# Performance work log

Measured on AMD Instinct MI355X. Metric: run time of the kernel, lower is better.

## Reference

```python
import jax, jax.numpy as jnp
import numpy as np

N_NODES = 100000
N_EDGES = 1600000
IN_DIM = 64
HID = 64
N_LAYERS = 2
BN_EPS = 1e-5


def setup_inputs() -> dict:
    key = jax.random.key(0)
    ks = jax.random.split(key, 10)
    s = 0.02
    return {
        "x": jax.random.normal(ks[0], (N_NODES, IN_DIM), dtype=jnp.float32),
        "edge_index": jax.random.randint(ks[1], (2, N_EDGES), 0, N_NODES),
        "edge_attr": jax.random.uniform(ks[2], (N_EDGES,), dtype=jnp.float32),
        "lin_W": jax.random.normal(ks[3], (IN_DIM, HID), dtype=jnp.float32) * s,
        "lin_b": jnp.zeros((HID,), dtype=jnp.float32),
        "eenc_w": jax.random.normal(ks[4], (HID,), dtype=jnp.float32) * s,
        "eenc_b": jnp.zeros((HID,), dtype=jnp.float32),
        "conv_W": jax.random.normal(ks[5], (N_LAYERS, HID, HID), dtype=jnp.float32) * s,
        "conv_b": jnp.zeros((N_LAYERS, HID), dtype=jnp.float32),
        "bn_gamma": jnp.ones((N_LAYERS, HID), dtype=jnp.float32),
        "bn_beta": jnp.zeros((N_LAYERS, HID), dtype=jnp.float32),
    }


def _forward(x, edge_index, edge_attr, lin_W, lin_b, eenc_w, eenc_b,
             conv_W, conv_b, bn_gamma, bn_beta):
    n = x.shape[0]
    src, dst = edge_index[0], edge_index[1]
    # input projection (in_dim > 1 -> lin_layer branch)
    h = x @ lin_W + lin_b                                  # [N, HID]
    e = edge_attr[:, None] * eenc_w[None, :] + eenc_b      # [E, HID]
    h0 = h
    h = h.at[src].set(jax.nn.relu(h0[src] + e))
    h = h.at[dst].set(jax.nn.relu(h0[dst] + e))
    # GCN normalization with self-loops (weight 1), shared across layers
    loops = jnp.arange(n)
    s2 = jnp.concatenate([src, loops])
    d2 = jnp.concatenate([dst, loops])
    w2 = jnp.concatenate([edge_attr, jnp.ones((n,), dtype=h.dtype)])
    deg = jax.ops.segment_sum(w2, d2, num_segments=n)
    dinv = jnp.where(deg > 0, 1.0 / jnp.sqrt(jnp.where(deg > 0, deg, 1.0)), 0.0)
    norm = dinv[s2] * w2 * dinv[d2]                        # [E+N]
    h_list = []
    for l in range(N_LAYERS):
        xw = h @ conv_W[l]                                 # [N, HID]
        agg = jax.ops.segment_sum(norm[:, None] * xw[s2], d2, num_segments=n)
        agg = agg + conv_b[l]
        mean = jnp.mean(agg, axis=0)
        var = jnp.mean((agg - mean) ** 2, axis=0)          # biased, as BN uses
        hn = (agg - mean) / jnp.sqrt(var + BN_EPS) * bn_gamma[l] + bn_beta[l]
        # dropout is identity (eval mode); relu on all but last layer
        h = hn if l == N_LAYERS - 1 else jax.nn.relu(hn)
        h_list.append(h)
    return jnp.concatenate(h_list, axis=1)                 # [N, N_LAYERS*HID]


def reference(x, edge_index, edge_attr, lin_W, lin_b, eenc_w, eenc_b,
              conv_W, conv_b, bn_gamma, bn_beta):
    return _forward(x, edge_index, edge_attr, lin_W, lin_b, eenc_w, eenc_b,
                    conv_W, conv_b, bn_gamma, bn_beta)
```

## Files before the change

kernel.cpp:

```cpp
#include <hip/hip_runtime.h>
#include <hip/hip_fp16.h>

#define N_NODES 100000
#define N_EDGES 1600000
#define BN_EPS 1e-5f
#define NBLK_E 6250
#define NBLK_G 3125
#define NBLK_N 391
#define NBINS 391
#define BCAP 4608
#define PT 4096
#define NPART 391
#define OVF_CAP 32768
#define A18 262144.0f
#define A18_INV 3.814697265625e-6f
typedef unsigned long long ull;
typedef unsigned int uint;


__global__ void init_kernel(int* gcnt, int* win, uint* zbitmap, int* flags, float* bnacc) {
    int v = blockIdx.x * blockDim.x + threadIdx.x;
    if (v < N_NODES) win[v] = -1;
    if (v < NBINS) gcnt[v] = 0;
    if (v < 3125) zbitmap[v] = 0;
    if (v < 2) flags[v] = 0;
    if (v < 256) bnacc[v] = 0.0f;
}

__launch_bounds__(256)
__global__ void partition_gemm(const int* __restrict__ src, const int* __restrict__ dst,
                               const float* __restrict__ attr,
                               ull* __restrict__ bucket, int* __restrict__ gcnt,
                               int* __restrict__ flags, int* __restrict__ ovf_b,
                               ull* __restrict__ ovf_e,
                               const float* __restrict__ x, const float* __restrict__ lin_W,
                               const float* __restrict__ lin_b, float* __restrict__ h0) {
    __shared__ ull ent[PT];
    __shared__ unsigned short ebin[PT];
    __shared__ int hist[NBINS];
    __shared__ int cur[NBINS];
    __shared__ int gdel[NBINS];
    __shared__ int sc[512];
    int t = threadIdx.x;
    if (blockIdx.x < NPART) {
        int e0 = blockIdx.x * PT;
        int n = N_EDGES - e0; if (n > PT) n = PT;
        for (int b = t; b < NBINS; b += 256) hist[b] = 0;
        __syncthreads();
        for (int k = t; k < n; k += 256) atomicAdd(&hist[dst[e0 + k] >> 8], 1);
        __syncthreads();
        sc[t] = (t < NBINS) ? hist[t] : 0;
        sc[t + 256] = (t + 256 < NBINS) ? hist[t + 256] : 0;
        __syncthreads();
        for (int off = 1; off < 512; off <<= 1) {
            int a0 = sc[t] + ((t >= off) ? sc[t - off] : 0);
            int a1 = sc[t + 256] + sc[t + 256 - off];
            __syncthreads();
            sc[t] = a0; sc[t + 256] = a1;
            __syncthreads();
        }
        for (int b = t; b < NBINS; b += 256) {
            int lb = sc[b] - hist[b];
            cur[b] = lb;
            int gb = atomicAdd(&gcnt[b], hist[b]);
            gdel[b] = gb - lb;
        }
        __syncthreads();
        for (int k = t; k < n; k += 256) {
            int i = e0 + k;
            int d = dst[i];
            uint aq = (uint)(attr[i] * A18); if (aq > 0x3FFFFu) aq = 0x3FFFFu;
            int bin = d >> 8;
            ull e = ((ull)(d & 255) << 56) | ((ull)i << 35) | ((ull)src[i] << 18) | aq;
            int p = atomicAdd(&cur[bin], 1);
            ent[p] = e;
            ebin[p] = (unsigned short)bin;
        }
        __syncthreads();
        for (int k = t; k < n; k += 256) {
            int b = ebin[k];
            int off = k + gdel[b];
            if (off < BCAP) bucket[(size_t)b * BCAP + off] = ent[k];
            else {
                int q = atomicAdd(&flags[1], 1);
                if (q < OVF_CAP) { ovf_b[q] = b; ovf_e[q] = ent[k]; }
            }
        }
        return;
    }
    float* xs = (float*)ent;
    int lane = t & 63, w = t >> 6;
    int base = (blockIdx.x - NPART) * 32;
    const float4* Xv = (const float4*)(x + (size_t)base * 64);
    float4* xsv = (float4*)xs;
    xsv[t] = Xv[t];
    xsv[t + 256] = Xv[t + 256];
    float wc[64];
    #pragma unroll
    for (int k = 0; k < 64; ++k) wc[k] = lin_W[k * 64 + lane];
    __syncthreads();
    float bval = lin_b[lane];
    for (int rr = 0; rr < 8; ++rr) {
        int rl = w * 8 + rr;
        float acc = bval;
        #pragma unroll
        for (int k = 0; k < 64; ++k) acc = fmaf(xs[rl * 64 + k], wc[k], acc);
        h0[(size_t)(base + rl) * 64 + lane] = acc;
    }
}

__launch_bounds__(256)
__global__ void finalize_reorder(const ull* __restrict__ bucket, const int* __restrict__ gcnt,
                                 const int* __restrict__ ovf_b, const ull* __restrict__ ovf_e,
                                 int* __restrict__ flags, uint* __restrict__ zbitmap,
                                 float* __restrict__ dinv, float* __restrict__ wa,
                                 ull* __restrict__ csr2, int* __restrict__ startv,
                                 int* __restrict__ lenv) {
    __shared__ ull ent[BCAP];
    __shared__ int cnt[256];
    __shared__ int sc[256];
    __shared__ int cur[256];
    __shared__ int cbase[257];
    int t = threadIdx.x, b = blockIdx.x;
    int len = gcnt[b], blen = len < BCAP ? len : BCAP;
    const ull* bb = bucket + (size_t)b * BCAP;
    cnt[t] = 0;
    __syncthreads();
    ull r[18];
    #pragma unroll
    for (int k = 0; k < 18; ++k) {
        int j = k * 256 + t;
        r[k] = 0;
        if (j < blen) {
            ull e = bb[j];
            r[k] = e;
            atomicAdd(&cnt[(int)(e >> 56)], 1);
        }
    }
    __syncthreads();
    sc[t] = cnt[t];
    __syncthreads();
    for (int off = 1; off < 256; off <<= 1) {
        int a = sc[t] + ((t >= off) ? sc[t - off] : 0);
        __syncthreads();
        sc[t] = a;
        __syncthreads();
    }
    cbase[t + 1] = sc[t];
    if (t == 0) cbase[0] = 0;
    cur[t] = sc[t] - cnt[t];
    __syncthreads();
    #pragma unroll
    for (int k = 0; k < 18; ++k) {
        int j = k * 256 + t;
        if (j < blen) {
            ull e = r[k];
            int p = atomicAdd(&cur[(int)(e >> 56)], 1);
            ent[p] = e;
        }
    }
    __syncthreads();
    size_t base = (size_t)b * BCAP;
    for (int k = t; k < blen; k += 256) {
        ull e = ent[k];
        csr2[base + k] = (((ull)(e & 0x3FFFFull)) << 32) | ((e >> 18) & 0x1FFFFull);
    }
    int j0 = cbase[t], j1 = cbase[t + 1];
    float sum = 0.0f; uint winx = 0, wat = 0;
    for (int j = j0; j < j1; ++j) {
        ull e = ent[j];
        uint aq = (uint)(e & 0x3FFFFull);
        sum += (float)aq * A18_INV;
        uint ei = (uint)((e >> 35) & 0x1FFFFFull) + 1u;
        if (ei > winx) { winx = ei; wat = aq; }
    }
    if (len > BCAP) {
        int oc = flags[1]; if (oc > OVF_CAP) oc = OVF_CAP;
        for (int q = 0; q < oc; ++q) {
            if (ovf_b[q] != b) continue;
            ull e = ovf_e[q];
            if ((int)(e >> 56) != t) continue;
            uint aq = (uint)(e & 0x3FFFFull);
            sum += (float)aq * A18_INV;
            uint ei = (uint)((e >> 35) & 0x1FFFFFull) + 1u;
            if (ei > winx) { winx = ei; wat = aq; }
        }
    }
    int v = b * 256 + t;
    if (v < N_NODES) {
        dinv[v] = rsqrtf(1.0f + sum);
        startv[v] = (int)(base + j0);
        lenv[v] = j1 - j0;
        if (winx > 0) {
            wa[v] = (float)wat * A18_INV;
        } else {
            wa[v] = -1.0f;
            atomicOr(&zbitmap[v >> 5], 1u << (v & 31));
            flags[0] = 1;
        }
    }
}

__global__ void fixup_scan(const int* __restrict__ src, const int* __restrict__ flags,
                           const uint* __restrict__ zbitmap, int* __restrict__ win) {
    if (flags[0] == 0) return;
    int i = blockIdx.x * 256 + threadIdx.x;
    int s = src[i];
    if ((zbitmap[s >> 5] >> (s & 31)) & 1u) atomicMax(&win[s], i);
}

__global__ void fixup_apply(const int* __restrict__ flags, const uint* __restrict__ zbitmap,
                            const int* __restrict__ win, const float* __restrict__ attr,
                            float* __restrict__ wa) {
    if (flags[0] == 0) return;
    int v = blockIdx.x * 256 + threadIdx.x;
    if (v >= N_NODES) return;
    if (((zbitmap[v >> 5] >> (v & 31)) & 1u) && win[v] >= 0) wa[v] = attr[win[v]];
}

__launch_bounds__(256)
__global__ void gemm_l0_nrm(const float* __restrict__ h0, const float* __restrict__ W,
                            const float* __restrict__ wa, const float* __restrict__ ew,
                            const float* __restrict__ eb, __half* __restrict__ xw16,
                            ull* __restrict__ csr2, const int* __restrict__ gcnt,
                            const float* __restrict__ dinv) {
    __shared__ float xs[2048];
    int t = threadIdx.x;
    if (blockIdx.x < NBINS) {
        int b = blockIdx.x;
        int len = gcnt[b], blen = len < BCAP ? len : BCAP;
        ull* c = csr2 + (size_t)b * BCAP;
        for (int k = t; k < blen; k += 256) {
            ull pk = c[k];
            uint s = (uint)pk;
            float np = (float)(uint)(pk >> 32) * A18_INV * dinv[s];
            c[k] = ((ull)__float_as_uint(np) << 32) | s;
        }
        return;
    }
    int lane = t & 63, w = t >> 6;
    int base = (blockIdx.x - NBINS) * 32;
    const float4* Hv = (const float4*)(h0 + (size_t)base * 64);
    #pragma unroll
    for (int q = 0; q < 2; ++q) {
        int idx = t + q * 256;
        int rl = idx >> 4, f0 = (idx & 15) * 4;
        float4 v = Hv[idx];
        float wav = wa[base + rl];
        if (wav >= 0.0f) {
            v.x = fmaxf(fmaf(wav, ew[f0 + 0], v.x + eb[f0 + 0]), 0.0f);
            v.y = fmaxf(fmaf(wav, ew[f0 + 1], v.y + eb[f0 + 1]), 0.0f);
            v.z = fmaxf(fmaf(wav, ew[f0 + 2], v.z + eb[f0 + 2]), 0.0f);
            v.w = fmaxf(fmaf(wav, ew[f0 + 3], v.w + eb[f0 + 3]), 0.0f);
        }
        ((float4*)xs)[idx] = v;
    }
    float wc[64];
    #pragma unroll
    for (int k = 0; k < 64; ++k) wc[k] = W[k * 64 + lane];
    __syncthreads();
    for (int rr = 0; rr < 8; ++rr) {
        int rl = w * 8 + rr;
        float acc = 0.0f;
        #pragma unroll
        for (int k = 0; k < 64; ++k) acc = fmaf(xs[rl * 64 + k], wc[k], acc);
        xw16[(size_t)(base + rl) * 64 + lane] = __float2half(acc);
    }
}

__launch_bounds__(256)
__global__ void gemm_l1(const float* __restrict__ agg, const float* __restrict__ bnacc,
                        const float* __restrict__ gamma, const float* __restrict__ beta,
                        const float* __restrict__ W, float* __restrict__ out,
                        __half* __restrict__ xw16) {
    __shared__ float xs[2048];
    int t = threadIdx.x, lane = t & 63, w = t >> 6;
    int base = blockIdx.x * 32;
    const float4* Av = (const float4*)(agg + (size_t)base * 64);
    const float invN = 1.0f / (float)N_NODES;
    #pragma unroll
    for (int q = 0; q < 2; ++q) {
        int idx = t + q * 256;
        int rl = idx >> 4, f0 = (idx & 15) * 4;
        float4 v = Av[idx];
        float vv[4] = {v.x, v.y, v.z, v.w};
        #pragma unroll
        for (int c = 0; c < 4; ++c) {
            int f = f0 + c;
            float mean = bnacc[f] * invN;
            float var = bnacc[64 + f] * invN - mean * mean;
            float scl = gamma[f] * rsqrtf(var + BN_EPS);
            float bs = beta[f] - mean * scl;
            vv[c] = fmaxf(fmaf(vv[c], scl, bs), 0.0f);
        }
        float4 r = {vv[0], vv[1], vv[2], vv[3]};
        ((float4*)xs)[idx] = r;
        *(float4*)(out + (size_t)(base + rl) * 128 + f0) = r;
    }
    float wc[64];
    #pragma unroll
    for (int k = 0; k < 64; ++k) wc[k] = W[k * 64 + lane];
    __syncthreads();
    for (int rr = 0; rr < 8; ++rr) {
        int rl = w * 8 + rr;
        float acc = 0.0f;
        #pragma unroll
        for (int k = 0; k < 64; ++k) acc = fmaf(xs[rl * 64 + k], wc[k], acc);
        xw16[(size_t)(base + rl) * 64 + lane] = __float2half(acc);
    }
}

__launch_bounds__(256)
__global__ void gather4(const __half* __restrict__ xw16, const ull* __restrict__ csr2,
                        const int* __restrict__ startv, const int* __restrict__ lenv,
                        const float* __restrict__ dinv, const int* __restrict__ gcnt,
                        const int* __restrict__ flags, const int* __restrict__ ovf_b,
                        const ull* __restrict__ ovf_e,
                        const float* __restrict__ convb, float* __restrict__ agg,
                        float* __restrict__ bnacc) {
    __shared__ float reds[4][64];
    __shared__ float redq[4][64];
    int t = threadIdx.x, lane = t & 63, w = t >> 6;
    int ng = lane >> 4, fl = lane & 15, f0 = fl * 4, ngb = ng << 4;
    float cb0 = convb[f0], cb1 = convb[f0 + 1], cb2 = convb[f0 + 2], cb3 = convb[f0 + 3];
    float s0 = 0.f, s1 = 0.f, s2 = 0.f, s3 = 0.f;
    float q0 = 0.f, q1 = 0.f, q2 = 0.f, q3 = 0.f;
    int ovfn = flags[1];
    for (int v = blockIdx.x * 16 + w * 4 + ng; v < N_NODES; v += 32768) {
        float dv = dinv[v];
        int sb = startv[v], ln = lenv[v];
        float2 raw = *(const float2*)(xw16 + (size_t)v * 64 + f0);
        float2 xv01 = __half22float2(*(__half2*)&raw.x);
        float2 xv23 = __half22float2(*(__half2*)&raw.y);
        float w2 = dv * dv;
        float a0 = w2 * xv01.x, a1 = w2 * xv01.y, a2 = w2 * xv23.x, a3 = w2 * xv23.y;
        float b0 = 0.f, b1 = 0.f, b2 = 0.f, b3 = 0.f;
        for (int c0 = 0; c0 < ln; c0 += 16) {
            int m = ln - c0; if (m > 16) m = 16;
            ull pk = (fl < m) ? csr2[sb + c0 + fl] : 0ull;
            int j = 0;
            for (; j + 4 <= m; j += 4) {
                ull pA = __shfl(pk, ngb + j, 64);
                ull pB = __shfl(pk, ngb + j + 1, 64);
                ull pC = __shfl(pk, ngb + j + 2, 64);
                ull pD = __shfl(pk, ngb + j + 3, 64);
                float2 rA = *(const float2*)(xw16 + (size_t)(uint)pA * 64 + f0);
                float2 rB = *(const float2*)(xw16 + (size_t)(uint)pB * 64 + f0);
                float2 rC = *(const float2*)(xw16 + (size_t)(uint)pC * 64 + f0);
                float2 rD = *(const float2*)(xw16 + (size_t)(uint)pD * 64 + f0);
                float nA = __uint_as_float((uint)(pA >> 32)) * dv;
                float nB = __uint_as_float((uint)(pB >> 32)) * dv;
                float nC = __uint_as_float((uint)(pC >> 32)) * dv;
                float nD = __uint_as_float((uint)(pD >> 32)) * dv;
                float2 xA01 = __half22float2(*(__half2*)&rA.x);
                float2 xA23 = __half22float2(*(__half2*)&rA.y);
                float2 xB01 = __half22float2(*(__half2*)&rB.x);
                float2 xB23 = __half22float2(*(__half2*)&rB.y);
                float2 xC01 = __half22float2(*(__half2*)&rC.x);
                float2 xC23 = __half22float2(*(__half2*)&rC.y);
                float2 xD01 = __half22float2(*(__half2*)&rD.x);
                float2 xD23 = __half22float2(*(__half2*)&rD.y);
                a0 = fmaf(nA, xA01.x, a0); a1 = fmaf(nA, xA01.y, a1);
                a2 = fmaf(nA, xA23.x, a2); a3 = fmaf(nA, xA23.y, a3);
                b0 = fmaf(nB, xB01.x, b0); b1 = fmaf(nB, xB01.y, b1);
                b2 = fmaf(nB, xB23.x, b2); b3 = fmaf(nB, xB23.y, b3);
                a0 = fmaf(nC, xC01.x, a0); a1 = fmaf(nC, xC01.y, a1);
                a2 = fmaf(nC, xC23.x, a2); a3 = fmaf(nC, xC23.y, a3);
                b0 = fmaf(nD, xD01.x, b0); b1 = fmaf(nD, xD01.y, b1);
                b2 = fmaf(nD, xD23.x, b2); b3 = fmaf(nD, xD23.y, b3);
            }
            for (; j < m; ++j) {
                ull pA = __shfl(pk, ngb + j, 64);
                float2 rA = *(const float2*)(xw16 + (size_t)(uint)pA * 64 + f0);
                float nA = __uint_as_float((uint)(pA >> 32)) * dv;
                float2 xA01 = __half22float2(*(__half2*)&rA.x);
                float2 xA23 = __half22float2(*(__half2*)&rA.y);
                a0 = fmaf(nA, xA01.x, a0); a1 = fmaf(nA, xA01.y, a1);
                a2 = fmaf(nA, xA23.x, a2); a3 = fmaf(nA, xA23.y, a3);
            }
        }
        float t0 = a0 + b0, t1 = a1 + b1, t2 = a2 + b2, t3 = a3 + b3;
        if (ovfn > 0 && gcnt[v >> 8] > BCAP) {
            int oc = ovfn; if (oc > OVF_CAP) oc = OVF_CAP;
            int ld = v & 255, b = v >> 8;
            for (int q = 0; q < oc; ++q) {
                if (ovf_b[q] != b) continue;
                ull e = ovf_e[q];
                if ((int)(e >> 56) != ld) continue;
                uint s = (uint)((e >> 18) & 0x1FFFFull);
                float nr = (float)(uint)(e & 0x3FFFFull) * A18_INV * dinv[s] * dv;
                float2 rr = *(const float2*)(xw16 + (size_t)s * 64 + f0);
                float2 x01 = __half22float2(*(__half2*)&rr.x);
                float2 x23 = __half22float2(*(__half2*)&rr.y);
                t0 = fmaf(nr, x01.x, t0); t1 = fmaf(nr, x01.y, t1);
                t2 = fmaf(nr, x23.x, t2); t3 = fmaf(nr, x23.y, t3);
            }
        }
        t0 += cb0; t1 += cb1; t2 += cb2; t3 += cb3;
        *(float4*)(agg + (size_t)v * 64 + f0) = make_float4(t0, t1, t2, t3);
        s0 += t0; q0 += t0 * t0;
        s1 += t1; q1 += t1 * t1;
        s2 += t2; q2 += t2 * t2;
        s3 += t3; q3 += t3 * t3;
    }
    s0 += __shfl_xor(s0, 16, 64); s0 += __shfl_xor(s0, 32, 64);
    s1 += __shfl_xor(s1, 16, 64); s1 += __shfl_xor(s1, 32, 64);
    s2 += __shfl_xor(s2, 16, 64); s2 += __shfl_xor(s2, 32, 64);
    s3 += __shfl_xor(s3, 16, 64); s3 += __shfl_xor(s3, 32, 64);
    q0 += __shfl_xor(q0, 16, 64); q0 += __shfl_xor(q0, 32, 64);
    q1 += __shfl_xor(q1, 16, 64); q1 += __shfl_xor(q1, 32, 64);
    q2 += __shfl_xor(q2, 16, 64); q2 += __shfl_xor(q2, 32, 64);
    q3 += __shfl_xor(q3, 16, 64); q3 += __shfl_xor(q3, 32, 64);
    if (ng == 0) {
        reds[w][f0] = s0; reds[w][f0 + 1] = s1; reds[w][f0 + 2] = s2; reds[w][f0 + 3] = s3;
        redq[w][f0] = q0; redq[w][f0 + 1] = q1; redq[w][f0 + 2] = q2; redq[w][f0 + 3] = q3;
    }
    __syncthreads();
    if (t < 64) {
        float ss = reds[0][t] + reds[1][t] + reds[2][t] + reds[3][t];
        float qq = redq[0][t] + redq[1][t] + redq[2][t] + redq[3][t];
        atomicAdd(&bnacc[t], ss);
        atomicAdd(&bnacc[64 + t], qq);
    }
}

__launch_bounds__(256)
__global__ void bn_final(const float* __restrict__ agg, const float* __restrict__ bnacc,
                         const float* __restrict__ gamma, const float* __restrict__ beta,
                         float* __restrict__ out) {
    int idx = blockIdx.x * 256 + threadIdx.x;
    int c = idx & 63, v = idx >> 6;
    const float invN = 1.0f / (float)N_NODES;
    float mean = bnacc[c] * invN;
    float var = bnacc[64 + c] * invN - mean * mean;
    float scl = gamma[c] * rsqrtf(var + BN_EPS);
    float bs = beta[c] - mean * scl;
    out[(size_t)v * 128 + 64 + c] = fmaf(agg[idx], scl, bs);
}

extern "C" void kernel_launch(void* const* d_in, const int* in_sizes, int n_in,
                              void* d_out, int out_size, void* d_ws, size_t ws_size,
                              hipStream_t stream) {
    const float* x      = (const float*)d_in[0];
    const int*   eidx   = (const int*)d_in[1];
    const float* attr   = (const float*)d_in[2];
    const float* lin_W  = (const float*)d_in[3];
    const float* lin_b  = (const float*)d_in[4];
    const float* eenc_w = (const float*)d_in[5];
    const float* eenc_b = (const float*)d_in[6];
    const float* conv_W = (const float*)d_in[7];
    const float* conv_b = (const float*)d_in[8];
    const float* gamma  = (const float*)d_in[9];
    const float* beta   = (const float*)d_in[10];
    float* out = (float*)d_out;

    const int* src = eidx;
    const int* dst = eidx + N_EDGES;

    char* p = (char*)d_ws;
    ull* bucket = (ull*)p;   p += (size_t)NBINS * BCAP * 8;
    ull* csr2   = (ull*)p;   p += (size_t)NBINS * BCAP * 8;
    ull* ovf_e  = (ull*)p;   p += (size_t)OVF_CAP * 8;
    float* h0   = (float*)p; p += (size_t)N_NODES * 64 * 4;
    __half* xw16 = (__half*)p; p += (size_t)N_NODES * 64 * 2;
    float* dinv = (float*)p; p += (size_t)N_NODES * 4;
    float* wa   = (float*)p; p += (size_t)N_NODES * 4;
    int* win    = (int*)p;   p += (size_t)N_NODES * 4;
    int* startv = (int*)p;   p += (size_t)N_NODES * 4;
    int* lenv   = (int*)p;   p += (size_t)N_NODES * 4;
    int* ovf_b  = (int*)p;   p += (size_t)OVF_CAP * 4;
    int* gcnt   = (int*)p;   p += (NBINS + 1) * 4 + 20;
    uint* zbitmap = (uint*)p; p += 3125 * 4 + 12;
    int* flags  = (int*)p;   p += 64;
    float* bnacc = (float*)p; p += 256 * 4;
    float* agg = h0;

    init_kernel<<<NBLK_N, 256, 0, stream>>>(gcnt, win, zbitmap, flags, bnacc);
    partition_gemm<<<NPART + NBLK_G, 256, 0, stream>>>(src, dst, attr, bucket, gcnt,
                                                       flags, ovf_b, ovf_e,
                                                       x, lin_W, lin_b, h0);
    finalize_reorder<<<NBINS, 256, 0, stream>>>(bucket, gcnt, ovf_b, ovf_e,
                                                flags, zbitmap, dinv, wa,
                                                csr2, startv, lenv);
    fixup_scan<<<NBLK_E, 256, 0, stream>>>(src, flags, zbitmap, win);
    fixup_apply<<<NBLK_N, 256, 0, stream>>>(flags, zbitmap, win, attr, wa);

    gemm_l0_nrm<<<NBINS + NBLK_G, 256, 0, stream>>>(h0, conv_W, wa, eenc_w, eenc_b,
                                                    xw16, csr2, gcnt, dinv);
    gather4<<<2048, 256, 0, stream>>>(xw16, csr2, startv, lenv, dinv, gcnt,
                                      flags, ovf_b, ovf_e, conv_b, agg, bnacc);
    gemm_l1<<<NBLK_G, 256, 0, stream>>>(agg, bnacc, gamma, beta,
                                        conv_W + 64 * 64, out, xw16);
    gather4<<<2048, 256, 0, stream>>>(xw16, csr2, startv, lenv, dinv, gcnt,
                                      flags, ovf_b, ovf_e, conv_b + 64, agg, bnacc + 128);
    bn_final<<<25000, 256, 0, stream>>>(agg, bnacc + 128, gamma + 64, beta + 64, out);
}
```

Baseline: 439.3 us.

## Restructure neighbor gather to 8 lanes per node with prefetched CSR chunks

The aggregation kernel now gives each node 8 lanes that each load 16 bytes of fp16 features, instead of 16 lanes loading 8 bytes. It launches exactly one node per lane group rather than using a grid-stride loop, and prefetches the next 8 CSR entries while the current 8 neighbour rows are loaded and accumulated in a fully unrolled loop. The aim is fewer, wider memory requests and more loads in flight per wave, for better latency hiding in the memory-bound gather. In exchange, padded slots are always processed: inactive entries point to node 0 with weight 0, which adds wasted loads for low-degree nodes and would turn into NaN if row 0 held non-finite values.

```diff
diff --git a/kernel.cpp b/kernel.cpp
--- a/kernel.cpp
+++ b/kernel.cpp
@@ -311,7 +311,7 @@
 }
 
 __launch_bounds__(256)
-__global__ void gather4(const __half* __restrict__ xw16, const ull* __restrict__ csr2,
+__global__ void gather8(const __half* __restrict__ xw16, const ull* __restrict__ csr2,
                         const int* __restrict__ startv, const int* __restrict__ lenv,
                         const float* __restrict__ dinv, const int* __restrict__ gcnt,
                         const int* __restrict__ flags, const int* __restrict__ ovf_b,
@@ -321,106 +321,94 @@
     __shared__ float reds[4][64];
     __shared__ float redq[4][64];
     int t = threadIdx.x, lane = t & 63, w = t >> 6;
-    int ng = lane >> 4, fl = lane & 15, f0 = fl * 4, ngb = ng << 4;
-    float cb0 = convb[f0], cb1 = convb[f0 + 1], cb2 = convb[f0 + 2], cb3 = convb[f0 + 3];
-    float s0 = 0.f, s1 = 0.f, s2 = 0.f, s3 = 0.f;
-    float q0 = 0.f, q1 = 0.f, q2 = 0.f, q3 = 0.f;
+    int ng = lane >> 3, fl = lane & 7, f0 = fl * 8, ngb = ng << 3;
+    int v = blockIdx.x * 32 + w * 8 + ng;
+    float dv = dinv[v];
+    int sb = startv[v], ln = lenv[v];
+    float4 raw = *(const float4*)(xw16 + (size_t)v * 64 + f0);
+    float w2 = dv * dv;
+    float acc[8];
+    {
+        const __half2* rh = (const __half2*)&raw;
+        #pragma unroll
+        for (int k = 0; k < 4; ++k) {
+            float2 f = __half22float2(rh[k]);
+            acc[2 * k] = w2 * f.x;
+            acc[2 * k + 1] = w2 * f.y;
+        }
+    }
+    ull pk = (fl < ln) ? csr2[sb + fl] : 0ull;
+    for (int c0 = 0; c0 < ln; c0 += 8) {
+        ull pkc = pk;
+        int rem = ln - c0 - 8;
+        pk = (fl < rem) ? csr2[sb + c0 + 8 + fl] : 0ull;
+        float nr[8];
+        float4 rw[8];
+        #pragma unroll
+        for (int j = 0; j < 8; ++j) {
+            ull pj = __shfl(pkc, ngb + j, 64);
+            nr[j] = __uint_as_float((uint)(pj >> 32)) * dv;
+            rw[j] = *(const float4*)(xw16 + (size_t)(uint)pj * 64 + f0);
+        }
+        #pragma unroll
+        for (int j = 0; j < 8; ++j) {
+            const __half2* rh = (const __half2*)&rw[j];
+            #pragma unroll
+            for (int k = 0; k < 4; ++k) {
+                float2 f = __half22float2(rh[k]);
+                acc[2 * k] = fmaf(nr[j], f.x, acc[2 * k]);
+                acc[2 * k + 1] = fmaf(nr[j], f.y, acc[2 * k + 1]);
+            }
+        }
+    }
     int ovfn = flags[1];
-    for (int v = blockIdx.x * 16 + w * 4 + ng; v < N_NODES; v += 32768) {
-        float dv = dinv[v];
-        int sb = startv[v], ln = lenv[v];
-        float2 raw = *(const float2*)(xw16 + (size_t)v * 64 + f0);
-        float2 xv01 = __half22float2(*(__half2*)&raw.x);
-        float2 xv23 = __half22float2(*(__half2*)&raw.y);
-        float w2 = dv * dv;
-        float a0 = w2 * xv01.x, a1 = w2 * xv01.y, a2 = w2 * xv23.x, a3 = w2 * xv23.y;
-        float b0 = 0.f, b1 = 0.f, b2 = 0.f, b3 = 0.f;
-        for (int c0 = 0; c0 < ln; c0 += 16) {
-            int m = ln - c0; if (m > 16) m = 16;
-            ull pk = (fl < m) ? csr2[sb + c0 + fl] : 0ull;
-            int j = 0;
-            for (; j + 4 <= m; j += 4) {
-                ull pA = __shfl(pk, ngb + j, 64);
-                ull pB = __shfl(pk, ngb + j + 1, 64);
-                ull pC = __shfl(pk, ngb + j + 2, 64);
-                ull pD = __shfl(pk, ngb + j + 3, 64);
-                float2 rA = *(const float2*)(xw16 + (size_t)(uint)pA * 64 + f0);
-                float2 rB = *(const float2*)(xw16 + (size_t)(uint)pB * 64 + f0);
-                float2 rC = *(const float2*)(xw16 + (size_t)(uint)pC * 64 + f0);
-                float2 rD = *(const float2*)(xw16 + (size_t)(uint)pD * 64 + f0);
-                float nA = __uint_as_float((uint)(pA >> 32)) * dv;
-                float nB = __uint_as_float((uint)(pB >> 32)) * dv;
-                float nC = __uint_as_float((uint)(pC >> 32)) * dv;
-                float nD = __uint_as_float((uint)(pD >> 32)) * dv;
-                float2 xA01 = __half22float2(*(__half2*)&rA.x);
-                float2 xA23 = __half22float2(*(__half2*)&rA.y);
-                float2 xB01 = __half22float2(*(__half2*)&rB.x);
-                float2 xB23 = __half22float2(*(__half2*)&rB.y);
-                float2 xC01 = __half22float2(*(__half2*)&rC.x);
-                float2 xC23 = __half22float2(*(__half2*)&rC.y);
-                float2 xD01 = __half22float2(*(__half2*)&rD.x);
-                float2 xD23 = __half22float2(*(__half2*)&rD.y);
-                a0 = fmaf(nA, xA01.x, a0); a1 = fmaf(nA, xA01.y, a1);
-                a2 = fmaf(nA, xA23.x, a2); a3 = fmaf(nA, xA23.y, a3);
-                b0 = fmaf(nB, xB01.x, b0); b1 = fmaf(nB, xB01.y, b1);
-                b2 = fmaf(nB, xB23.x, b2); b3 = fmaf(nB, xB23.y, b3);
-                a0 = fmaf(nC, xC01.x, a0); a1 = fmaf(nC, xC01.y, a1);
-                a2 = fmaf(nC, xC23.x, a2); a3 = fmaf(nC, xC23.y, a3);
-                b0 = fmaf(nD, xD01.x, b0); b1 = fmaf(nD, xD01.y, b1);
-                b2 = fmaf(nD, xD23.x, b2); b3 = fmaf(nD, xD23.y, b3);
+    if (ovfn > 0 && gcnt[v >> 8] > BCAP) {
+        int oc = ovfn; if (oc > OVF_CAP) oc = OVF_CAP;
+        int ld = v & 255, b = v >> 8;
+        for (int q = 0; q < oc; ++q) {
+            if (ovf_b[q] != b) continue;
+            ull e = ovf_e[q];
+            if ((int)(e >> 56) != ld) continue;
+            uint s = (uint)((e >> 18) & 0x1FFFFull);
+            float nrx = (float)(uint)(e & 0x3FFFFull) * A18_INV * dinv[s] * dv;
+            float4 rr = *(const float4*)(xw16 + (size_t)s * 64 + f0);
+            const __half2* rh = (const __half2*)&rr;
+            #pragma unroll
+            for (int k = 0; k < 4; ++k) {
+                float2 f = __half22float2(rh[k]);
+                acc[2 * k] = fmaf(nrx, f.x, acc[2 * k]);
+                acc[2 * k + 1] = fmaf(nrx, f.y, acc[2 * k + 1]);
             }
-            for (; j < m; ++j) {
-                ull pA = __shfl(pk, ngb + j, 64);
-                float2 rA = *(const float2*)(xw16 + (size_t)(uint)pA * 64 + f0);
-                float nA = __uint_as_float((uint)(pA >> 32)) * dv;
-                float2 xA01 = __half22float2(*(__half2*)&rA.x);
-                float2 xA23 = __half22float2(*(__half2*)&rA.y);
-                a0 = fmaf(nA, xA01.x, a0); a1 = fmaf(nA, xA01.y, a1);
-                a2 = fmaf(nA, xA23.x, a2); a3 = fmaf(nA, xA23.y, a3);
-            }
-        }
-        float t0 = a0 + b0, t1 = a1 + b1, t2 = a2 + b2, t3 = a3 + b3;
-        if (ovfn > 0 && gcnt[v >> 8] > BCAP) {
-            int oc = ovfn; if (oc > OVF_CAP) oc = OVF_CAP;
-            int ld = v & 255, b = v >> 8;
-            for (int q = 0; q < oc; ++q) {
-                if (ovf_b[q] != b) continue;
-                ull e = ovf_e[q];
-                if ((int)(e >> 56) != ld) continue;
-                uint s = (uint)((e >> 18) & 0x1FFFFull);
-                float nr = (float)(uint)(e & 0x3FFFFull) * A18_INV * dinv[s] * dv;
-                float2 rr = *(const float2*)(xw16 + (size_t)s * 64 + f0);
-                float2 x01 = __half22float2(*(__half2*)&rr.x);
-                float2 x23 = __half22float2(*(__half2*)&rr.y);
-                t0 = fmaf(nr, x01.x, t0); t1 = fmaf(nr, x01.y, t1);
-                t2 = fmaf(nr, x23.x, t2); t3 = fmaf(nr, x23.y, t3);
-            }
-        }
-        t0 += cb0; t1 += cb1; t2 += cb2; t3 += cb3;
-        *(float4*)(agg + (size_t)v * 64 + f0) = make_float4(t0, t1, t2, t3);
-        s0 += t0; q0 += t0 * t0;
-        s1 += t1; q1 += t1 * t1;
-        s2 += t2; q2 += t2 * t2;
-        s3 += t3; q3 += t3 * t3;
-    }
-    s0 += __shfl_xor(s0, 16, 64); s0 += __shfl_xor(s0, 32, 64);
-    s1 += __shfl_xor(s1, 16, 64); s1 += __shfl_xor(s1, 32, 64);
-    s2 += __shfl_xor(s2, 16, 64); s2 += __shfl_xor(s2, 32, 64);
-    s3 += __shfl_xor(s3, 16, 64); s3 += __shfl_xor(s3, 32, 64);
-    q0 += __shfl_xor(q0, 16, 64); q0 += __shfl_xor(q0, 32, 64);
-    q1 += __shfl_xor(q1, 16, 64); q1 += __shfl_xor(q1, 32, 64);
-    q2 += __shfl_xor(q2, 16, 64); q2 += __shfl_xor(q2, 32, 64);
-    q3 += __shfl_xor(q3, 16, 64); q3 += __shfl_xor(q3, 32, 64);
+        }
+    }
+    float4 cbA = *(const float4*)(convb + f0);
+    float4 cbB = *(const float4*)(convb + f0 + 4);
+    acc[0] += cbA.x; acc[1] += cbA.y; acc[2] += cbA.z; acc[3] += cbA.w;
+    acc[4] += cbB.x; acc[5] += cbB.y; acc[6] += cbB.z; acc[7] += cbB.w;
+    *(float4*)(agg + (size_t)v * 64 + f0) = make_float4(acc[0], acc[1], acc[2], acc[3]);
+    *(float4*)(agg + (size_t)v * 64 + f0 + 4) = make_float4(acc[4], acc[5], acc[6], acc[7]);
+    float ss[8], qq[8];
+    #pragma unroll
+    for (int k = 0; k < 8; ++k) { ss[k] = acc[k]; qq[k] = acc[k] * acc[k]; }
+    #pragma unroll
+    for (int k = 0; k < 8; ++k) {
+        ss[k] += __shfl_xor(ss[k], 8, 64);
+        ss[k] += __shfl_xor(ss[k], 16, 64);
+        ss[k] += __shfl_xor(ss[k], 32, 64);
+        qq[k] += __shfl_xor(qq[k], 8, 64);
+        qq[k] += __shfl_xor(qq[k], 16, 64);
+        qq[k] += __shfl_xor(qq[k], 32, 64);
+    }
     if (ng == 0) {
-        reds[w][f0] = s0; reds[w][f0 + 1] = s1; reds[w][f0 + 2] = s2; reds[w][f0 + 3] = s3;
-        redq[w][f0] = q0; redq[w][f0 + 1] = q1; redq[w][f0 + 2] = q2; redq[w][f0 + 3] = q3;
+        #pragma unroll
+        for (int k = 0; k < 8; ++k) { reds[w][f0 + k] = ss[k]; redq[w][f0 + k] = qq[k]; }
     }
     __syncthreads();
     if (t < 64) {
-        float ss = reds[0][t] + reds[1][t] + reds[2][t] + reds[3][t];
-        float qq = redq[0][t] + redq[1][t] + redq[2][t] + redq[3][t];
-        atomicAdd(&bnacc[t], ss);
-        atomicAdd(&bnacc[64 + t], qq);
+        float s4 = reds[0][t] + reds[1][t] + reds[2][t] + reds[3][t];
+        float q4 = redq[0][t] + redq[1][t] + redq[2][t] + redq[3][t];
+        atomicAdd(&bnacc[t], s4);
+        atomicAdd(&bnacc[64 + t], q4);
     }
 }
 
@@ -487,11 +475,11 @@
 
     gemm_l0_nrm<<<NBINS + NBLK_G, 256, 0, stream>>>(h0, conv_W, wa, eenc_w, eenc_b,
                                                     xw16, csr2, gcnt, dinv);
-    gather4<<<2048, 256, 0, stream>>>(xw16, csr2, startv, lenv, dinv, gcnt,
-                                      flags, ovf_b, ovf_e, conv_b, agg, bnacc);
+    gather8<<<NBLK_G, 256, 0, stream>>>(xw16, csr2, startv, lenv, dinv, gcnt,
+                                        flags, ovf_b, ovf_e, conv_b, agg, bnacc);
     gemm_l1<<<NBLK_G, 256, 0, stream>>>(agg, bnacc, gamma, beta,
                                         conv_W + 64 * 64, out, xw16);
-    gather4<<<2048, 256, 0, stream>>>(xw16, csr2, startv, lenv, dinv, gcnt,
-                                      flags, ovf_b, ovf_e, conv_b + 64, agg, bnacc + 128);
+    gather8<<<NBLK_G, 256, 0, stream>>>(xw16, csr2, startv, lenv, dinv, gcnt,
+                                        flags, ovf_b, ovf_e, conv_b + 64, agg, bnacc + 128);
     bn_final<<<25000, 256, 0, stream>>>(agg, bnacc + 128, gamma + 64, beta + 64, out);
 }
```

Result: slower. 468.3 us (+6.6%).

## Restructure gather to one node per lane group with prefetch and full unroll

Applied to the files above, without the earlier changes.

The grid-stride gather kernel is replaced by one that assigns exactly one destination node to each 16-lane group, launched with enough blocks to cover all nodes. Each group prefetches the next chunk of CSR entries while processing the current one, and unrolls all 16 neighbour loads so more independent memory requests are in flight. Padded lanes read row 0 with zero weight, which wastes some loads on partially filled chunks. More blocks also means more atomic updates to the BN accumulators.

```diff
diff --git a/kernel.cpp b/kernel.cpp
--- a/kernel.cpp
+++ b/kernel.cpp
@@ -310,99 +310,75 @@
     }
 }
 
-__launch_bounds__(256)
-__global__ void gather4(const __half* __restrict__ xw16, const ull* __restrict__ csr2,
-                        const int* __restrict__ startv, const int* __restrict__ lenv,
-                        const float* __restrict__ dinv, const int* __restrict__ gcnt,
-                        const int* __restrict__ flags, const int* __restrict__ ovf_b,
-                        const ull* __restrict__ ovf_e,
-                        const float* __restrict__ convb, float* __restrict__ agg,
-                        float* __restrict__ bnacc) {
+__launch_bounds__(256, 2)
+__global__ void gather16(const __half* __restrict__ xw16, const ull* __restrict__ csr2,
+                         const int* __restrict__ startv, const int* __restrict__ lenv,
+                         const float* __restrict__ dinv, const int* __restrict__ gcnt,
+                         const int* __restrict__ flags, const int* __restrict__ ovf_b,
+                         const ull* __restrict__ ovf_e,
+                         const float* __restrict__ convb, float* __restrict__ agg,
+                         float* __restrict__ bnacc) {
     __shared__ float reds[4][64];
     __shared__ float redq[4][64];
     int t = threadIdx.x, lane = t & 63, w = t >> 6;
     int ng = lane >> 4, fl = lane & 15, f0 = fl * 4, ngb = ng << 4;
-    float cb0 = convb[f0], cb1 = convb[f0 + 1], cb2 = convb[f0 + 2], cb3 = convb[f0 + 3];
-    float s0 = 0.f, s1 = 0.f, s2 = 0.f, s3 = 0.f;
-    float q0 = 0.f, q1 = 0.f, q2 = 0.f, q3 = 0.f;
+    int v = blockIdx.x * 16 + w * 4 + ng;
+    float dv = dinv[v];
+    int sb = startv[v], ln = lenv[v];
+    float2 raw = *(const float2*)(xw16 + (size_t)v * 64 + f0);
+    float2 xv01 = __half22float2(*(__half2*)&raw.x);
+    float2 xv23 = __half22float2(*(__half2*)&raw.y);
+    float w2 = dv * dv;
+    float a0 = w2 * xv01.x, a1 = w2 * xv01.y, a2 = w2 * xv23.x, a3 = w2 * xv23.y;
+    float b0 = 0.f, b1 = 0.f, b2 = 0.f, b3 = 0.f;
+    ull pk = (fl < ln) ? csr2[sb + fl] : 0ull;
+    for (int c0 = 0; c0 < ln; c0 += 16) {
+        ull pkc = pk;
+        int rem = ln - c0 - 16;
+        pk = (fl < rem) ? csr2[sb + c0 + 16 + fl] : 0ull;
+        float nr[16];
+        float2 rw[16];
+        #pragma unroll
+        for (int j = 0; j < 16; ++j) {
+            ull pj = __shfl(pkc, ngb + j, 64);
+            nr[j] = __uint_as_float((uint)(pj >> 32)) * dv;
+            rw[j] = *(const float2*)(xw16 + (size_t)(uint)pj * 64 + f0);
+        }
+        #pragma unroll
+        for (int j = 0; j < 16; j += 2) {
+            float2 xA01 = __half22float2(*(__half2*)&rw[j].x);
+            float2 xA23 = __half22float2(*(__half2*)&rw[j].y);
+            float2 xB01 = __half22float2(*(__half2*)&rw[j + 1].x);
+            float2 xB23 = __half22float2(*(__half2*)&rw[j + 1].y);
+            a0 = fmaf(nr[j], xA01.x, a0); a1 = fmaf(nr[j], xA01.y, a1);
+            a2 = fmaf(nr[j], xA23.x, a2); a3 = fmaf(nr[j], xA23.y, a3);
+            b0 = fmaf(nr[j + 1], xB01.x, b0); b1 = fmaf(nr[j + 1], xB01.y, b1);
+            b2 = fmaf(nr[j + 1], xB23.x, b2); b3 = fmaf(nr[j + 1], xB23.y, b3);
+        }
+    }
+    float t0 = a0 + b0, t1 = a1 + b1, t2 = a2 + b2, t3 = a3 + b3;
     int ovfn = flags[1];
-    for (int v = blockIdx.x * 16 + w * 4 + ng; v < N_NODES; v += 32768) {
-        float dv = dinv[v];
-        int sb = startv[v], ln = lenv[v];
-        float2 raw = *(const float2*)(xw16 + (size_t)v * 64 + f0);
-        float2 xv01 = __half22float2(*(__half2*)&raw.x);
-        float2 xv23 = __half22float2(*(__half2*)&raw.y);
-        float w2 = dv * dv;
-        float a0 = w2 * xv01.x, a1 = w2 * xv01.y, a2 = w2 * xv23.x, a3 = w2 * xv23.y;
-        float b0 = 0.f, b1 = 0.f, b2 = 0.f, b3 = 0.f;
-        for (int c0 = 0; c0 < ln; c0 += 16) {
-            int m = ln - c0; if (m > 16) m = 16;
-            ull pk = (fl < m) ? csr2[sb + c0 + fl] : 0ull;
-            int j = 0;
-            for (; j + 4 <= m; j += 4) {
-                ull pA = __shfl(pk, ngb + j, 64);
-                ull pB = __shfl(pk, ngb + j + 1, 64);
-                ull pC = __shfl(pk, ngb + j + 2, 64);
-                ull pD = __shfl(pk, ngb + j + 3, 64);
-                float2 rA = *(const float2*)(xw16 + (size_t)(uint)pA * 64 + f0);
-                float2 rB = *(const float2*)(xw16 + (size_t)(uint)pB * 64 + f0);
-                float2 rC = *(const float2*)(xw16 + (size_t)(uint)pC * 64 + f0);
-                float2 rD = *(const float2*)(xw16 + (size_t)(uint)pD * 64 + f0);
-                float nA = __uint_as_float((uint)(pA >> 32)) * dv;
-                float nB = __uint_as_float((uint)(pB >> 32)) * dv;
-                float nC = __uint_as_float((uint)(pC >> 32)) * dv;
-                float nD = __uint_as_float((uint)(pD >> 32)) * dv;
-                float2 xA01 = __half22float2(*(__half2*)&rA.x);
-                float2 xA23 = __half22float2(*(__half2*)&rA.y);
-                float2 xB01 = __half22float2(*(__half2*)&rB.x);
-                float2 xB23 = __half22float2(*(__half2*)&rB.y);
-                float2 xC01 = __half22float2(*(__half2*)&rC.x);
-                float2 xC23 = __half22float2(*(__half2*)&rC.y);
-                float2 xD01 = __half22float2(*(__half2*)&rD.x);
-                float2 xD23 = __half22float2(*(__half2*)&rD.y);
-                a0 = fmaf(nA, xA01.x, a0); a1 = fmaf(nA, xA01.y, a1);
-                a2 = fmaf(nA, xA23.x, a2); a3 = fmaf(nA, xA23.y, a3);
-                b0 = fmaf(nB, xB01.x, b0); b1 = fmaf(nB, xB01.y, b1);
-                b2 = fmaf(nB, xB23.x, b2); b3 = fmaf(nB, xB23.y, b3);
-                a0 = fmaf(nC, xC01.x, a0); a1 = fmaf(nC, xC01.y, a1);
-                a2 = fmaf(nC, xC23.x, a2); a3 = fmaf(nC, xC23.y, a3);
-                b0 = fmaf(nD, xD01.x, b0); b1 = fmaf(nD, xD01.y, b1);
-                b2 = fmaf(nD, xD23.x, b2); b3 = fmaf(nD, xD23.y, b3);
-            }
-            for (; j < m; ++j) {
-                ull pA = __shfl(pk, ngb + j, 64);
-                float2 rA = *(const float2*)(xw16 + (size_t)(uint)pA * 64 + f0);
-                float nA = __uint_as_float((uint)(pA >> 32)) * dv;
-                float2 xA01 = __half22float2(*(__half2*)&rA.x);
-                float2 xA23 = __half22float2(*(__half2*)&rA.y);
-                a0 = fmaf(nA, xA01.x, a0); a1 = fmaf(nA, xA01.y, a1);
-                a2 = fmaf(nA, xA23.x, a2); a3 = fmaf(nA, xA23.y, a3);
-            }
-        }
-        float t0 = a0 + b0, t1 = a1 + b1, t2 = a2 + b2, t3 = a3 + b3;
-        if (ovfn > 0 && gcnt[v >> 8] > BCAP) {
-            int oc = ovfn; if (oc > OVF_CAP) oc = OVF_CAP;
-            int ld = v & 255, b = v >> 8;
-            for (int q = 0; q < oc; ++q) {
-                if (ovf_b[q] != b) continue;
-                ull e = ovf_e[q];
-                if ((int)(e >> 56) != ld) continue;
-                uint s = (uint)((e >> 18) & 0x1FFFFull);
-                float nr = (float)(uint)(e & 0x3FFFFull) * A18_INV * dinv[s] * dv;
-                float2 rr = *(const float2*)(xw16 + (size_t)s * 64 + f0);
-                float2 x01 = __half22float2(*(__half2*)&rr.x);
-                float2 x23 = __half22float2(*(__half2*)&rr.y);
-                t0 = fmaf(nr, x01.x, t0); t1 = fmaf(nr, x01.y, t1);
-                t2 = fmaf(nr, x23.x, t2); t3 = fmaf(nr, x23.y, t3);
-            }
-        }
-        t0 += cb0; t1 += cb1; t2 += cb2; t3 += cb3;
-        *(float4*)(agg + (size_t)v * 64 + f0) = make_float4(t0, t1, t2, t3);
-        s0 += t0; q0 += t0 * t0;
-        s1 += t1; q1 += t1 * t1;
-        s2 += t2; q2 += t2 * t2;
-        s3 += t3; q3 += t3 * t3;
-    }
+    if (ovfn > 0 && gcnt[v >> 8] > BCAP) {
+        int oc = ovfn; if (oc > OVF_CAP) oc = OVF_CAP;
+        int ld = v & 255, b = v >> 8;
+        for (int q = 0; q < oc; ++q) {
+            if (ovf_b[q] != b) continue;
+            ull e = ovf_e[q];
+            if ((int)(e >> 56) != ld) continue;
+            uint s = (uint)((e >> 18) & 0x1FFFFull);
+            float nrx = (float)(uint)(e & 0x3FFFFull) * A18_INV * dinv[s] * dv;
+            float2 rr = *(const float2*)(xw16 + (size_t)s * 64 + f0);
+            float2 x01 = __half22float2(*(__half2*)&rr.x);
+            float2 x23 = __half22float2(*(__half2*)&rr.y);
+            t0 = fmaf(nrx, x01.x, t0); t1 = fmaf(nrx, x01.y, t1);
+            t2 = fmaf(nrx, x23.x, t2); t3 = fmaf(nrx, x23.y, t3);
+        }
+    }
+    float4 cb = *(const float4*)(convb + f0);
+    t0 += cb.x; t1 += cb.y; t2 += cb.z; t3 += cb.w;
+    *(float4*)(agg + (size_t)v * 64 + f0) = make_float4(t0, t1, t2, t3);
+    float s0 = t0, s1 = t1, s2 = t2, s3 = t3;
+    float q0 = t0 * t0, q1 = t1 * t1, q2 = t2 * t2, q3 = t3 * t3;
     s0 += __shfl_xor(s0, 16, 64); s0 += __shfl_xor(s0, 32, 64);
     s1 += __shfl_xor(s1, 16, 64); s1 += __shfl_xor(s1, 32, 64);
     s2 += __shfl_xor(s2, 16, 64); s2 += __shfl_xor(s2, 32, 64);
@@ -487,11 +463,11 @@
 
     gemm_l0_nrm<<<NBINS + NBLK_G, 256, 0, stream>>>(h0, conv_W, wa, eenc_w, eenc_b,
                                                     xw16, csr2, gcnt, dinv);
-    gather4<<<2048, 256, 0, stream>>>(xw16, csr2, startv, lenv, dinv, gcnt,
-                                      flags, ovf_b, ovf_e, conv_b, agg, bnacc);
+    gather16<<<6250, 256, 0, stream>>>(xw16, csr2, startv, lenv, dinv, gcnt,
+                                       flags, ovf_b, ovf_e, conv_b, agg, bnacc);
     gemm_l1<<<NBLK_G, 256, 0, stream>>>(agg, bnacc, gamma, beta,
                                         conv_W + 64 * 64, out, xw16);
-    gather4<<<2048, 256, 0, stream>>>(xw16, csr2, startv, lenv, dinv, gcnt,
-                                      flags, ovf_b, ovf_e, conv_b + 64, agg, bnacc + 128);
+    gather16<<<6250, 256, 0, stream>>>(xw16, csr2, startv, lenv, dinv, gcnt,
+                                       flags, ovf_b, ovf_e, conv_b + 64, agg, bnacc + 128);
     bn_final<<<25000, 256, 0, stream>>>(agg, bnacc + 128, gamma + 64, beta + 64, out);
 }
```

Result: slower. 661.8 us (+50.6%).
